# Performance work log

Measured on AMD Instinct MI355X. Metric: run time of the kernel, lower is better.

Reference implementation:

```python
import jax, jax.numpy as jnp
import numpy as np

B, S, D, H = 2, 2048, 2048, 16
HD = D // H  # head_dim = 128
ALIBI_BIAS_MAX = 8


def alibi_bias(n_heads, seq_len, alibi_bias_max=8, dtype=jnp.float32):
    # matches torch alibi_bias(full=False): shape [1, H, 1, S]
    dist = jnp.arange(1 - seq_len, 1, dtype=dtype).reshape(1, 1, 1, seq_len)
    m = jnp.arange(1, n_heads + 1, dtype=dtype) * (alibi_bias_max / n_heads)
    slopes = (1.0 / 2.0 ** m).reshape(1, n_heads, 1, 1)
    return dist * slopes


def setup_inputs() -> dict:
    key = jax.random.key(0)
    k1, k2, k3, k4, k5 = jax.random.split(key, 5)
    x = jax.random.normal(k1, (B, S, D), dtype=jnp.float32)
    # ALiBi additive bias, as produced by TritonFlashCausalAttention.attn_mask_
    attn_mask = alibi_bias(H, S, ALIBI_BIAS_MAX, jnp.float32)  # [1,H,1,S]
    scale = 1.0 / np.sqrt(D)
    Wqkv = jax.random.normal(k2, (D, 3 * D), dtype=jnp.float32) * scale
    bqkv = jnp.zeros((3 * D,), dtype=jnp.float32)
    Wout = jax.random.normal(k3, (D, D), dtype=jnp.float32) * scale
    bout = jnp.zeros((D,), dtype=jnp.float32)
    return {"x": x, "attn_mask": attn_mask, "Wqkv": Wqkv, "bqkv": bqkv,
            "Wout": Wout, "bout": bout}


def reference(x, attn_mask, Wqkv, bqkv, Wout, bout):
    b, s, d = x.shape
    # fused QKV projection
    qkv = x @ Wqkv + bqkv                       # [B,S,3D]
    qkv = qkv.reshape(b, s, 3, H, HD)
    q, k, v = qkv[:, :, 0], qkv[:, :, 1], qkv[:, :, 2]  # each [B,S,H,HD]
    softmax_scale = 1.0 / jnp.sqrt(jnp.asarray(HD, dtype=x.dtype))
    scores = jnp.einsum('bshd,bthd->bhst', q, k) * softmax_scale  # [B,H,S,S]
    scores = scores + attn_mask                  # ALiBi bias [1,H,1,S]
    causal = jnp.tril(jnp.ones((s, s), dtype=bool))
    scores = jnp.where(causal, scores, jnp.asarray(-jnp.inf, dtype=scores.dtype))
    attn = jax.nn.softmax(scores, axis=-1)
    out = jnp.einsum('bhst,bthd->bshd', attn, v).reshape(b, s, d)
    return out @ Wout + bout
```

## Files before the change

### kernel.cpp

```cpp
#include <hip/hip_runtime.h>
#include <hip/hip_bf16.h>

typedef __bf16 bf16x8 __attribute__((ext_vector_type(8)));
typedef float f32x4 __attribute__((ext_vector_type(4)));
typedef unsigned short u16;

constexpr int BATCH = 2, SEQ = 2048, DM = 2048, NH = 16, HD = 128;
constexpr int N3 = 3 * DM;
constexpr int MROWS = BATCH * SEQ;

__device__ __forceinline__ u16 f2bf(float f) {
  unsigned u = __builtin_bit_cast(unsigned, f);
  unsigned r = 0x7FFFu + ((u >> 16) & 1u);
  return (u16)((u + r) >> 16);
}

__device__ __forceinline__ void glds16(const u16* g, u16* l) {
  __builtin_amdgcn_global_load_lds(
      (const __attribute__((address_space(1))) unsigned*)(const void*)g,
      (__attribute__((address_space(3))) unsigned*)(void*)l, 16, 0, 0);
}

__global__ __launch_bounds__(256) void k_cvt(const float* __restrict__ in,
                                             u16* __restrict__ out, int n4) {
  int i = blockIdx.x * blockDim.x + threadIdx.x;
  if (i >= n4) return;
  float4 v = reinterpret_cast<const float4*>(in)[i];
  ushort4 o;
  o.x = f2bf(v.x); o.y = f2bf(v.y); o.z = f2bf(v.z); o.w = f2bf(v.w);
  reinterpret_cast<ushort4*>(out)[i] = o;
}

__global__ __launch_bounds__(256) void k_transpose(const float* __restrict__ in,
                                                   u16* __restrict__ out, int K, int N) {
  __shared__ float tile[32][33];
  int n0 = blockIdx.x * 32, k0 = blockIdx.y * 32;
  int tx = threadIdx.x & 31, ty = threadIdx.x >> 5;
#pragma unroll
  for (int r = ty; r < 32; r += 8) tile[r][tx] = in[(long)(k0 + r) * N + n0 + tx];
  __syncthreads();
#pragma unroll
  for (int r = ty; r < 32; r += 8) out[(long)(n0 + r) * K + k0 + tx] = f2bf(tile[tx][r]);
}

__global__ __launch_bounds__(256, 2) void k_gemm_qkv(const u16* __restrict__ A,
                                                     const u16* __restrict__ Bt,
                                                     const float* __restrict__ bias,
                                                     u16* __restrict__ Qb, u16* __restrict__ Kb,
                                                     u16* __restrict__ Vt) {
  constexpr int K = DM;
  constexpr int NKT = K / 64;
  constexpr int NIT = NKT / 2;
  __shared__ u16 LA[2 * 128 * 64];
  __shared__ u16 LB[2 * 192 * 64];
  int m0 = blockIdx.y * 128, n0 = blockIdx.x * 192;
  int t = threadIdx.x, lane = t & 63, w = t >> 6;
  int l15 = lane & 15, lhi = lane >> 4;
  int wrow = w >> 1, wcol = w & 1;
  int srow = t >> 3;
  int scol = ((t & 7) ^ (srow & 7)) * 8;

#define STG_A(TILE, IDX) do {                                                      \
    int kb_ = ((TILE) < NKT ? (TILE) : NKT - 1) * 64;                              \
    glds16(A + (long)(m0 + (IDX) * 32 + srow) * K + kb_ + scol,                    \
           LA + ((TILE) & 1) * 8192 + (IDX) * 2048 + w * 512);                     \
  } while (0)
#define STG_B(TILE, IDX) do {                                                      \
    int kb_ = ((TILE) < NKT ? (TILE) : NKT - 1) * 64;                              \
    glds16(Bt + (long)(n0 + (IDX) * 32 + srow) * K + kb_ + scol,                   \
           LB + ((TILE) & 1) * 12288 + (IDX) * 2048 + w * 512);                    \
  } while (0)

  bf16x8 af[2][2], bfr0[3][2], bfr1[3][2];
  f32x4 acc[4][6] = {};

#define LDA_FRAGS(BUF, QM) do {                                                    \
    _Pragma("unroll") for (int mi = 0; mi < 2; mi++) {                             \
      int rA = wrow * 64 + ((QM) * 2 + mi) * 16 + l15;                             \
      _Pragma("unroll") for (int kk = 0; kk < 2; kk++)                             \
        af[mi][kk] = *(const bf16x8*)(LA + (BUF) * 8192 + rA * 64 +                \
                                      (((kk * 4 + lhi) ^ (rA & 7)) * 8));          \
    } } while (0)
#define LDB_FRAGS(BUF, QN, DST) do {                                               \
    _Pragma("unroll") for (int ni = 0; ni < 3; ni++) {                             \
      int rB = wcol * 96 + ((QN) * 3 + ni) * 16 + l15;                             \
      _Pragma("unroll") for (int kk = 0; kk < 2; kk++)                             \
        DST[ni][kk] = *(const bf16x8*)(LB + (BUF) * 12288 + rB * 64 +              \
                                       (((kk * 4 + lhi) ^ (rB & 7)) * 8));         \
    } } while (0)
#define MM(QM, QN, BF) do {                                                        \
    __builtin_amdgcn_s_setprio(1);                                                 \
    _Pragma("unroll") for (int mi = 0; mi < 2; mi++)                               \
    _Pragma("unroll") for (int ni = 0; ni < 3; ni++)                               \
    _Pragma("unroll") for (int kk = 0; kk < 2; kk++)                               \
      acc[(QM) * 2 + mi][(QN) * 3 + ni] = __builtin_amdgcn_mfma_f32_16x16x32_bf16( \
          af[mi][kk], BF[ni][kk], acc[(QM) * 2 + mi][(QN) * 3 + ni], 0, 0, 0);     \
    __builtin_amdgcn_s_setprio(0);                                                 \
  } while (0)
#define BAR __builtin_amdgcn_s_barrier()
#define LG0 do { asm volatile("s_waitcnt lgkmcnt(0)" ::: "memory");                \
                 __builtin_amdgcn_sched_barrier(0); } while (0)
#define VMW6 do { asm volatile("s_waitcnt vmcnt(6)" ::: "memory");                 \
                  __builtin_amdgcn_sched_barrier(0); } while (0)

  STG_A(0, 0); STG_A(0, 1); STG_A(0, 2); STG_A(0, 3);
  STG_B(0, 0); STG_B(0, 1); STG_B(0, 2); STG_B(0, 3); STG_B(0, 4); STG_B(0, 5);
  STG_B(1, 0); STG_B(1, 1); STG_B(1, 2); STG_B(1, 3); STG_B(1, 4); STG_B(1, 5);
  VMW6; BAR;

  for (int it = 0; it < NIT; it++) {
    int k1 = 2 * it + 1, k2 = 2 * it + 2, k3 = 2 * it + 3;
    LDA_FRAGS(0, 0); LDB_FRAGS(0, 0, bfr0);
    STG_A(k1, 0); STG_A(k1, 1); STG_A(k1, 2);      BAR; LG0; MM(0, 0, bfr0); BAR;
    LDB_FRAGS(0, 1, bfr1);
    STG_A(k1, 3);                                  BAR; LG0; MM(0, 1, bfr1); BAR;
    LDA_FRAGS(0, 1);
    STG_B(k2, 0); STG_B(k2, 1); STG_B(k2, 2);      BAR; LG0; MM(1, 0, bfr0); BAR;
    STG_B(k2, 3); STG_B(k2, 4); STG_B(k2, 5);
    VMW6;                                          BAR;      MM(1, 1, bfr1); BAR;
    LDA_FRAGS(1, 0); LDB_FRAGS(1, 0, bfr0);
    STG_A(k2, 0); STG_A(k2, 1); STG_A(k2, 2);      BAR; LG0; MM(0, 0, bfr0); BAR;
    LDB_FRAGS(1, 1, bfr1);
    STG_A(k2, 3);                                  BAR; LG0; MM(0, 1, bfr1); BAR;
    LDA_FRAGS(1, 1);
    STG_B(k3, 0); STG_B(k3, 1); STG_B(k3, 2);      BAR; LG0; MM(1, 0, bfr0); BAR;
    STG_B(k3, 3); STG_B(k3, 4); STG_B(k3, 5);
    VMW6;                                          BAR;      MM(1, 1, bfr1); BAR;
  }
#undef STG_A
#undef STG_B
#undef LDA_FRAGS
#undef LDB_FRAGS
#undef MM
#undef BAR
#undef LG0
#undef VMW6

#pragma unroll
  for (int mi = 0; mi < 4; mi++)
#pragma unroll
    for (int ni = 0; ni < 6; ni++) {
      int col = n0 + wcol * 96 + ni * 16 + l15;
      float bv = bias[col];
      int sec = col >> 11, dn = col & 2047, h = dn >> 7, hd = dn & 127;
#pragma unroll
      for (int r = 0; r < 4; r++) {
        int row = m0 + wrow * 64 + mi * 16 + lhi * 4 + r;
        int bb = row >> 11, ss = row & 2047;
        u16 val = f2bf(acc[mi][ni][r] + bv);
        if (sec == 0)
          Qb[(((long)(bb * NH + h)) * SEQ + ss) * HD + hd] = val;
        else if (sec == 1)
          Kb[(((long)(bb * NH + h)) * SEQ + ss) * HD + hd] = val;
        else
          Vt[(((long)(bb * NH + h)) * HD + hd) * SEQ + ss] = val;
      }
    }
}

__global__ __launch_bounds__(256) void k_gemm_out(const u16* __restrict__ A,
                                                  const u16* __restrict__ Bt,
                                                  const float* __restrict__ bias,
                                                  float* __restrict__ Out) {
  constexpr int K = DM, N = DM;
  __shared__ u16 As[128 * 32], Bs[128 * 32];
  int m0 = blockIdx.y * 128, n0 = blockIdx.x * 128;
  int t = threadIdx.x, lane = t & 63, w = t >> 6;
  int l15 = lane & 15, lhi = lane >> 4;
  int wr = (w >> 1) * 64, wc = (w & 1) * 64;
  int srow = t >> 2, sk = (t & 3) * 8;
  const u16* Ap0 = A + (long)(m0 + srow) * K + sk;
  const u16* Ap1 = A + (long)(m0 + 64 + srow) * K + sk;
  const u16* Bp0 = Bt + (long)(n0 + srow) * K + sk;
  const u16* Bp1 = Bt + (long)(n0 + 64 + srow) * K + sk;
  u16* AsW0 = As + w * 512; u16* AsW1 = As + 2048 + w * 512;
  u16* BsW0 = Bs + w * 512; u16* BsW1 = Bs + 2048 + w * 512;

  f32x4 acc[4][4] = {};
  for (int k0 = 0; k0 < K; k0 += 32) {
    glds16(Ap0 + k0, AsW0);
    glds16(Ap1 + k0, AsW1);
    glds16(Bp0 + k0, BsW0);
    glds16(Bp1 + k0, BsW1);
    __syncthreads();
    bf16x8 af[4], bg[4];
#pragma unroll
    for (int i = 0; i < 4; i++) af[i] = *(const bf16x8*)(As + (wr + i * 16 + l15) * 32 + lhi * 8);
#pragma unroll
    for (int j = 0; j < 4; j++) bg[j] = *(const bf16x8*)(Bs + (wc + j * 16 + l15) * 32 + lhi * 8);
#pragma unroll
    for (int i = 0; i < 4; i++)
#pragma unroll
      for (int j = 0; j < 4; j++)
        acc[i][j] = __builtin_amdgcn_mfma_f32_16x16x32_bf16(af[i], bg[j], acc[i][j], 0, 0, 0);
    __syncthreads();
  }
#pragma unroll
  for (int i = 0; i < 4; i++)
#pragma unroll
    for (int j = 0; j < 4; j++) {
      int col = n0 + wc + j * 16 + l15;
      float bv = bias[col];
#pragma unroll
      for (int r = 0; r < 4; r++) {
        int row = m0 + wr + i * 16 + lhi * 4 + r;
        Out[(long)row * N + col] = acc[i][j][r] + bv;
      }
    }
}

__global__ __launch_bounds__(256) void k_attn(const u16* __restrict__ Qb,
                                              const u16* __restrict__ Kb,
                                              const u16* __restrict__ Vt,
                                              const float* __restrict__ mask,
                                              u16* __restrict__ Ao) {
  constexpr int NT = SEQ / 64;
  int bh = blockIdx.y;
  int qp = blockIdx.x;
  int t = threadIdx.x, w = t >> 6, lane = t & 63;
  int l15 = lane & 15, lhi = lane >> 4;
  int b = bh >> 4, h = bh & 15;
  const u16* Qh = Qb + (long)bh * SEQ * HD;
  const u16* Kh = Kb + (long)bh * SEQ * HD;
  const u16* Vh = Vt + (long)bh * HD * SEQ;
  const float* mh = mask + h * SEQ;

  __shared__ u16 Ks[64 * 128];
  __shared__ u16 Vs[128 * 64];
  __shared__ u16 p_lds[4 * 16 * 64];
  u16* pw = p_lds + w * (16 * 64);

  int krow[4], kcol[4], vrow[4], vcol[4];
#pragma unroll
  for (int i = 0; i < 4; i++) {
    int c = i * 256 + t;
    krow[i] = c >> 4; kcol[i] = (c & 15) * 8;
    vrow[i] = c >> 3; vcol[i] = (c & 7) * 8;
  }

  const float sm_scale = 0.08838834764831845f;

  for (int half = 0; half < 2; half++) {
    int qt = half ? qp : (NT - 1 - qp);
    int q0 = qt * 64 + w * 16;
    int nt = qt + 1;

    bf16x8 qf[4];
#pragma unroll
    for (int kc = 0; kc < 4; kc++)
      qf[kc] = *(const bf16x8*)(Qh + (long)(q0 + l15) * HD + kc * 32 + lhi * 8);

    int rowr[4];
#pragma unroll
    for (int r = 0; r < 4; r++) rowr[r] = q0 + lhi * 4 + r;

    float mrun[4], lrun[4];
    f32x4 oacc[8] = {};
#pragma unroll
    for (int r = 0; r < 4; r++) { mrun[r] = -1e30f; lrun[r] = 0.f; }

    bf16x8 kst[4], vst[4];
#pragma unroll
    for (int i = 0; i < 4; i++) kst[i] = *(const bf16x8*)(Kh + (long)krow[i] * HD + kcol[i]);
#pragma unroll
    for (int i = 0; i < 4; i++) vst[i] = *(const bf16x8*)(Vh + (long)vrow[i] * SEQ + vcol[i]);
    __syncthreads();
#pragma unroll
    for (int i = 0; i < 4; i++)
      *(bf16x8*)(Ks + krow[i] * 128 + (kcol[i] ^ ((krow[i] & 7) << 3))) = kst[i];
#pragma unroll
    for (int i = 0; i < 4; i++)
      *(bf16x8*)(Vs + vrow[i] * 64 + (vcol[i] ^ ((vrow[i] & 7) << 3))) = vst[i];
    __syncthreads();

    for (int kt = 0; kt < nt; kt++) {
      int kb = kt * 64;
      bool have_next = (kt + 1 < nt);
      bool diag = (kt == nt - 1);
      if (have_next) {
        int kb2 = kb + 64;
#pragma unroll
        for (int i = 0; i < 4; i++)
          kst[i] = *(const bf16x8*)(Kh + (long)(kb2 + krow[i]) * HD + kcol[i]);
#pragma unroll
        for (int i = 0; i < 4; i++)
          vst[i] = *(const bf16x8*)(Vh + (long)vrow[i] * SEQ + kb2 + vcol[i]);
      }
      float bvv[4];
#pragma unroll
      for (int cb = 0; cb < 4; cb++) bvv[cb] = mh[kb + cb * 16 + l15];
      f32x4 sc[4] = {};
      __builtin_amdgcn_s_setprio(1);
#pragma unroll
      for (int kc = 0; kc < 4; kc++)
#pragma unroll
        for (int cb = 0; cb < 4; cb++) {
          int rr = cb * 16 + l15;
          bf16x8 kf = *(const bf16x8*)(Ks + rr * 128 + ((kc * 32 + lhi * 8) ^ ((rr & 7) << 3)));
          sc[cb] = __builtin_amdgcn_mfma_f32_16x16x32_bf16(qf[kc], kf, sc[cb], 0, 0, 0);
        }
      __builtin_amdgcn_s_setprio(0);
      float p[4][4], tmax[4];
#pragma unroll
      for (int cb = 0; cb < 4; cb++) {
        int col = kb + cb * 16 + l15;
#pragma unroll
        for (int r = 0; r < 4; r++) {
          float v = sc[cb][r] * sm_scale + bvv[cb];
          if (diag) v = (col <= rowr[r]) ? v : -1e30f;
          p[cb][r] = v;
        }
      }
#pragma unroll
      for (int r = 0; r < 4; r++)
        tmax[r] = fmaxf(fmaxf(p[0][r], p[1][r]), fmaxf(p[2][r], p[3][r]));
      float alpha[4];
#pragma unroll
      for (int r = 0; r < 4; r++) {
        float v = tmax[r];
        v = fmaxf(v, __shfl_xor(v, 1));
        v = fmaxf(v, __shfl_xor(v, 2));
        v = fmaxf(v, __shfl_xor(v, 4));
        v = fmaxf(v, __shfl_xor(v, 8));
        float mnew = fmaxf(mrun[r], v);
        alpha[r] = __expf(mrun[r] - mnew);
        mrun[r] = mnew;
        float s = 0.f;
#pragma unroll
        for (int cb = 0; cb < 4; cb++) {
          float e = __expf(p[cb][r] - mnew);
          p[cb][r] = e;
          s += e;
        }
        s += __shfl_xor(s, 1); s += __shfl_xor(s, 2);
        s += __shfl_xor(s, 4); s += __shfl_xor(s, 8);
        lrun[r] = lrun[r] * alpha[r] + s;
      }
#pragma unroll
      for (int nb = 0; nb < 8; nb++)
#pragma unroll
        for (int r = 0; r < 4; r++) oacc[nb][r] *= alpha[r];
#pragma unroll
      for (int cb = 0; cb < 4; cb++)
#pragma unroll
        for (int r = 0; r < 4; r++) {
          int rr = lhi * 4 + r;
          pw[(rr * 64 + cb * 16 + l15) ^ ((rr & 7) << 3)] = f2bf(p[cb][r]);
        }
      asm volatile("s_waitcnt lgkmcnt(0)" ::: "memory");
      bf16x8 pa0 = *(const bf16x8*)(pw + ((l15 * 64 + lhi * 8) ^ ((l15 & 7) << 3)));
      bf16x8 pa1 = *(const bf16x8*)(pw + ((l15 * 64 + 32 + lhi * 8) ^ ((l15 & 7) << 3)));
      __builtin_amdgcn_s_setprio(1);
#pragma unroll
      for (int nb = 0; nb < 8; nb++) {
        int rr = nb * 16 + l15;
        bf16x8 vf0 = *(const bf16x8*)(Vs + rr * 64 + ((lhi * 8) ^ ((rr & 7) << 3)));
        bf16x8 vf1 = *(const bf16x8*)(Vs + rr * 64 + ((32 + lhi * 8) ^ ((rr & 7) << 3)));
        oacc[nb] = __builtin_amdgcn_mfma_f32_16x16x32_bf16(pa0, vf0, oacc[nb], 0, 0, 0);
        oacc[nb] = __builtin_amdgcn_mfma_f32_16x16x32_bf16(pa1, vf1, oacc[nb], 0, 0, 0);
      }
      __builtin_amdgcn_s_setprio(0);
      if (have_next) {
        __syncthreads();
#pragma unroll
        for (int i = 0; i < 4; i++)
          *(bf16x8*)(Ks + krow[i] * 128 + (kcol[i] ^ ((krow[i] & 7) << 3))) = kst[i];
#pragma unroll
        for (int i = 0; i < 4; i++)
          *(bf16x8*)(Vs + vrow[i] * 64 + (vcol[i] ^ ((vrow[i] & 7) << 3))) = vst[i];
        __syncthreads();
      }
    }
#pragma unroll
    for (int nb = 0; nb < 8; nb++)
#pragma unroll
      for (int r = 0; r < 4; r++) {
        int row = q0 + lhi * 4 + r;
        float v = oacc[nb][r] / lrun[r];
        Ao[((long)(b * SEQ + row)) * DM + h * HD + nb * 16 + l15] = f2bf(v);
      }
  }
}

extern "C" void kernel_launch(void* const* d_in, const int* in_sizes, int n_in,
                              void* d_out, int out_size, void* d_ws, size_t ws_size,
                              hipStream_t stream) {
  const float* x    = (const float*)d_in[0];
  const float* amsk = (const float*)d_in[1];
  const float* Wqkv = (const float*)d_in[2];
  const float* bqkv = (const float*)d_in[3];
  const float* Wout = (const float*)d_in[4];
  const float* bout = (const float*)d_in[5];
  float* out = (float*)d_out;

  char* ws = (char*)d_ws;
  u16* xb  = (u16*)(ws + 0);
  u16* WqT = (u16*)(ws + 16777216UL);
  u16* WoT = (u16*)(ws + 41943040UL);
  u16* Qb  = (u16*)(ws + 50331648UL);
  u16* Kb  = (u16*)(ws + 67108864UL);
  u16* Vt  = (u16*)(ws + 83886080UL);
  u16* Ao  = (u16*)(ws + 100663296UL);

  k_cvt<<<8192, 256, 0, stream>>>(x, xb, (MROWS * DM) / 4);
  k_transpose<<<dim3(N3 / 32, DM / 32), 256, 0, stream>>>(Wqkv, WqT, DM, N3);
  k_transpose<<<dim3(DM / 32, DM / 32), 256, 0, stream>>>(Wout, WoT, DM, DM);
  k_gemm_qkv<<<dim3(N3 / 192, MROWS / 128), 256, 0, stream>>>(xb, WqT, bqkv, Qb, Kb, Vt);
  k_attn<<<dim3(SEQ / 128, BATCH * NH), 256, 0, stream>>>(Qb, Kb, Vt, amsk, Ao);
  k_gemm_out<<<dim3(DM / 128, MROWS / 128), 256, 0, stream>>>(Ao, WoT, bout, out);
}
```

Baseline: 296.3 us.

## Split attention KV loop across two wave groups with final softmax merge

The attention kernel now launches 512 threads per block, organised as two groups of four waves. Each group processes alternate 64-key tiles into its own K/V shared buffers, which splits the sequential KV loop for each query tile in half. At the end, group 1 writes its partial output, max and sum to shared memory, and group 0 merges the two online-softmax states before writing. The goal is more parallelism per block, since the grid has only 512 blocks. The cost is double the shared memory, extra barriers, and merge overhead. Occupancy may also be limited by launch_bounds(512,4) register pressure.

```diff
diff --git a/kernel.cpp b/kernel.cpp
--- a/kernel.cpp
+++ b/kernel.cpp
@@ -209,31 +209,35 @@
     }
 }
 
-__global__ __launch_bounds__(256) void k_attn(const u16* __restrict__ Qb,
-                                              const u16* __restrict__ Kb,
-                                              const u16* __restrict__ Vt,
-                                              const float* __restrict__ mask,
-                                              u16* __restrict__ Ao) {
+__global__ __launch_bounds__(512, 4) void k_attn(const u16* __restrict__ Qb,
+                                                 const u16* __restrict__ Kb,
+                                                 const u16* __restrict__ Vt,
+                                                 const float* __restrict__ mask,
+                                                 u16* __restrict__ Ao) {
   constexpr int NT = SEQ / 64;
   int bh = blockIdx.y;
   int qp = blockIdx.x;
   int t = threadIdx.x, w = t >> 6, lane = t & 63;
+  int g = w >> 2, wi = w & 3;
   int l15 = lane & 15, lhi = lane >> 4;
+  int tg = t & 255;
   int b = bh >> 4, h = bh & 15;
   const u16* Qh = Qb + (long)bh * SEQ * HD;
   const u16* Kh = Kb + (long)bh * SEQ * HD;
   const u16* Vh = Vt + (long)bh * HD * SEQ;
   const float* mh = mask + h * SEQ;
 
-  __shared__ u16 Ks[64 * 128];
-  __shared__ u16 Vs[128 * 64];
-  __shared__ u16 p_lds[4 * 16 * 64];
+  __shared__ u16 Ks[2][64 * 128];
+  __shared__ u16 Vs[2][128 * 64];
+  __shared__ u16 p_lds[8 * 16 * 64];
   u16* pw = p_lds + w * (16 * 64);
+  u16* Ksg = Ks[g];
+  u16* Vsg = Vs[g];
 
   int krow[4], kcol[4], vrow[4], vcol[4];
 #pragma unroll
   for (int i = 0; i < 4; i++) {
-    int c = i * 256 + t;
+    int c = i * 256 + tg;
     krow[i] = c >> 4; kcol[i] = (c & 15) * 8;
     vrow[i] = c >> 3; vcol[i] = (c & 7) * 8;
   }
@@ -242,43 +246,46 @@
 
   for (int half = 0; half < 2; half++) {
     int qt = half ? qp : (NT - 1 - qp);
-    int q0 = qt * 64 + w * 16;
+    int q0 = qt * 64 + wi * 16;
     int nt = qt + 1;
+    int nIt = (nt + 1) >> 1;
 
     bf16x8 qf[4];
 #pragma unroll
     for (int kc = 0; kc < 4; kc++)
       qf[kc] = *(const bf16x8*)(Qh + (long)(q0 + l15) * HD + kc * 32 + lhi * 8);
 
-    int rowr[4];
-#pragma unroll
-    for (int r = 0; r < 4; r++) rowr[r] = q0 + lhi * 4 + r;
-
     float mrun[4], lrun[4];
     f32x4 oacc[8] = {};
 #pragma unroll
     for (int r = 0; r < 4; r++) { mrun[r] = -1e30f; lrun[r] = 0.f; }
 
     bf16x8 kst[4], vst[4];
-#pragma unroll
-    for (int i = 0; i < 4; i++) kst[i] = *(const bf16x8*)(Kh + (long)krow[i] * HD + kcol[i]);
-#pragma unroll
-    for (int i = 0; i < 4; i++) vst[i] = *(const bf16x8*)(Vh + (long)vrow[i] * SEQ + vcol[i]);
-    __syncthreads();
-#pragma unroll
-    for (int i = 0; i < 4; i++)
-      *(bf16x8*)(Ks + krow[i] * 128 + (kcol[i] ^ ((krow[i] & 7) << 3))) = kst[i];
-#pragma unroll
-    for (int i = 0; i < 4; i++)
-      *(bf16x8*)(Vs + vrow[i] * 64 + (vcol[i] ^ ((vrow[i] & 7) << 3))) = vst[i];
-    __syncthreads();
-
-    for (int kt = 0; kt < nt; kt++) {
+    if (g < nt) {
+      int kb0 = g * 64;
+#pragma unroll
+      for (int i = 0; i < 4; i++) kst[i] = *(const bf16x8*)(Kh + (long)(kb0 + krow[i]) * HD + kcol[i]);
+#pragma unroll
+      for (int i = 0; i < 4; i++) vst[i] = *(const bf16x8*)(Vh + (long)vrow[i] * SEQ + kb0 + vcol[i]);
+    }
+    __syncthreads();
+    if (g < nt) {
+#pragma unroll
+      for (int i = 0; i < 4; i++)
+        *(bf16x8*)(Ksg + krow[i] * 128 + (kcol[i] ^ ((krow[i] & 7) << 3))) = kst[i];
+#pragma unroll
+      for (int i = 0; i < 4; i++)
+        *(bf16x8*)(Vsg + vrow[i] * 64 + (vcol[i] ^ ((vrow[i] & 7) << 3))) = vst[i];
+    }
+    __syncthreads();
+
+    for (int it = 0; it < nIt; it++) {
+      int kt = 2 * it + g;
+      bool active = kt < nt;
       int kb = kt * 64;
-      bool have_next = (kt + 1 < nt);
-      bool diag = (kt == nt - 1);
-      if (have_next) {
-        int kb2 = kb + 64;
+      bool havenext = (kt + 2) < nt;
+      if (havenext) {
+        int kb2 = kb + 128;
 #pragma unroll
         for (int i = 0; i < 4; i++)
           kst[i] = *(const bf16x8*)(Kh + (long)(kb2 + krow[i]) * HD + kcol[i]);
@@ -286,99 +293,134 @@
         for (int i = 0; i < 4; i++)
           vst[i] = *(const bf16x8*)(Vh + (long)vrow[i] * SEQ + kb2 + vcol[i]);
       }
-      float bvv[4];
-#pragma unroll
-      for (int cb = 0; cb < 4; cb++) bvv[cb] = mh[kb + cb * 16 + l15];
-      f32x4 sc[4] = {};
-      __builtin_amdgcn_s_setprio(1);
-#pragma unroll
-      for (int kc = 0; kc < 4; kc++)
+      if (active) {
+        bool diag = (kt == nt - 1);
+        float bvv[4];
+#pragma unroll
+        for (int cb = 0; cb < 4; cb++) bvv[cb] = mh[kb + cb * 16 + l15];
+        f32x4 sc[4] = {};
+        __builtin_amdgcn_s_setprio(1);
+#pragma unroll
+        for (int kc = 0; kc < 4; kc++)
+#pragma unroll
+          for (int cb = 0; cb < 4; cb++) {
+            int rr = cb * 16 + l15;
+            bf16x8 kf = *(const bf16x8*)(Ksg + rr * 128 + ((kc * 32 + lhi * 8) ^ ((rr & 7) << 3)));
+            sc[cb] = __builtin_amdgcn_mfma_f32_16x16x32_bf16(qf[kc], kf, sc[cb], 0, 0, 0);
+          }
+        __builtin_amdgcn_s_setprio(0);
+        float p[4][4], tmax[4];
 #pragma unroll
         for (int cb = 0; cb < 4; cb++) {
-          int rr = cb * 16 + l15;
-          bf16x8 kf = *(const bf16x8*)(Ks + rr * 128 + ((kc * 32 + lhi * 8) ^ ((rr & 7) << 3)));
-          sc[cb] = __builtin_amdgcn_mfma_f32_16x16x32_bf16(qf[kc], kf, sc[cb], 0, 0, 0);
-        }
-      __builtin_amdgcn_s_setprio(0);
-      float p[4][4], tmax[4];
-#pragma unroll
-      for (int cb = 0; cb < 4; cb++) {
-        int col = kb + cb * 16 + l15;
+          int col = kb + cb * 16 + l15;
+#pragma unroll
+          for (int r = 0; r < 4; r++) {
+            float v = sc[cb][r] * sm_scale + bvv[cb];
+            if (diag) v = (col <= q0 + lhi * 4 + r) ? v : -1e30f;
+            p[cb][r] = v;
+          }
+        }
+#pragma unroll
+        for (int r = 0; r < 4; r++)
+          tmax[r] = fmaxf(fmaxf(p[0][r], p[1][r]), fmaxf(p[2][r], p[3][r]));
+        float alpha[4];
 #pragma unroll
         for (int r = 0; r < 4; r++) {
-          float v = sc[cb][r] * sm_scale + bvv[cb];
-          if (diag) v = (col <= rowr[r]) ? v : -1e30f;
-          p[cb][r] = v;
-        }
-      }
-#pragma unroll
-      for (int r = 0; r < 4; r++)
-        tmax[r] = fmaxf(fmaxf(p[0][r], p[1][r]), fmaxf(p[2][r], p[3][r]));
-      float alpha[4];
+          float v = tmax[r];
+          v = fmaxf(v, __shfl_xor(v, 1));
+          v = fmaxf(v, __shfl_xor(v, 2));
+          v = fmaxf(v, __shfl_xor(v, 4));
+          v = fmaxf(v, __shfl_xor(v, 8));
+          float mnew = fmaxf(mrun[r], v);
+          alpha[r] = __expf(mrun[r] - mnew);
+          mrun[r] = mnew;
+          float s = 0.f;
+#pragma unroll
+          for (int cb = 0; cb < 4; cb++) {
+            float e = __expf(p[cb][r] - mnew);
+            p[cb][r] = e;
+            s += e;
+          }
+          s += __shfl_xor(s, 1); s += __shfl_xor(s, 2);
+          s += __shfl_xor(s, 4); s += __shfl_xor(s, 8);
+          lrun[r] = lrun[r] * alpha[r] + s;
+        }
+#pragma unroll
+        for (int nb = 0; nb < 8; nb++)
+#pragma unroll
+          for (int r = 0; r < 4; r++) oacc[nb][r] *= alpha[r];
+#pragma unroll
+        for (int cb = 0; cb < 4; cb++)
+#pragma unroll
+          for (int r = 0; r < 4; r++) {
+            int rr = lhi * 4 + r;
+            pw[(rr * 64 + cb * 16 + l15) ^ ((rr & 7) << 3)] = f2bf(p[cb][r]);
+          }
+        asm volatile("s_waitcnt lgkmcnt(0)" ::: "memory");
+        bf16x8 pa0 = *(const bf16x8*)(pw + ((l15 * 64 + lhi * 8) ^ ((l15 & 7) << 3)));
+        bf16x8 pa1 = *(const bf16x8*)(pw + ((l15 * 64 + 32 + lhi * 8) ^ ((l15 & 7) << 3)));
+        __builtin_amdgcn_s_setprio(1);
+#pragma unroll
+        for (int nb = 0; nb < 8; nb++) {
+          int rr = nb * 16 + l15;
+          bf16x8 vf0 = *(const bf16x8*)(Vsg + rr * 64 + ((lhi * 8) ^ ((rr & 7) << 3)));
+          bf16x8 vf1 = *(const bf16x8*)(Vsg + rr * 64 + ((32 + lhi * 8) ^ ((rr & 7) << 3)));
+          oacc[nb] = __builtin_amdgcn_mfma_f32_16x16x32_bf16(pa0, vf0, oacc[nb], 0, 0, 0);
+          oacc[nb] = __builtin_amdgcn_mfma_f32_16x16x32_bf16(pa1, vf1, oacc[nb], 0, 0, 0);
+        }
+        __builtin_amdgcn_s_setprio(0);
+      }
+      if (it + 1 < nIt) {
+        __syncthreads();
+        if (havenext) {
+#pragma unroll
+          for (int i = 0; i < 4; i++)
+            *(bf16x8*)(Ksg + krow[i] * 128 + (kcol[i] ^ ((krow[i] & 7) << 3))) = kst[i];
+#pragma unroll
+          for (int i = 0; i < 4; i++)
+            *(bf16x8*)(Vsg + vrow[i] * 64 + (vcol[i] ^ ((vrow[i] & 7) << 3))) = vst[i];
+        }
+        __syncthreads();
+      }
+    }
+
+    __syncthreads();
+    float* KsF = (float*)&Ks[0][0];
+    float* plF = (float*)p_lds;
+    if (g == 1) {
+#pragma unroll
+      for (int nb = 0; nb < 8; nb++)
+#pragma unroll
+        for (int r = 0; r < 4; r++)
+          KsF[wi * 2048 + (lhi * 4 + r) * 128 + nb * 16 + l15] = oacc[nb][r];
+      if (l15 == 0) {
+#pragma unroll
+        for (int r = 0; r < 4; r++) {
+          plF[wi * 32 + (lhi * 4 + r) * 2 + 0] = mrun[r];
+          plF[wi * 32 + (lhi * 4 + r) * 2 + 1] = lrun[r];
+        }
+      }
+    }
+    __syncthreads();
+    if (g == 0) {
 #pragma unroll
       for (int r = 0; r < 4; r++) {
-        float v = tmax[r];
-        v = fmaxf(v, __shfl_xor(v, 1));
-        v = fmaxf(v, __shfl_xor(v, 2));
-        v = fmaxf(v, __shfl_xor(v, 4));
-        v = fmaxf(v, __shfl_xor(v, 8));
-        float mnew = fmaxf(mrun[r], v);
-        alpha[r] = __expf(mrun[r] - mnew);
-        mrun[r] = mnew;
-        float s = 0.f;
-#pragma unroll
-        for (int cb = 0; cb < 4; cb++) {
-          float e = __expf(p[cb][r] - mnew);
-          p[cb][r] = e;
-          s += e;
-        }
-        s += __shfl_xor(s, 1); s += __shfl_xor(s, 2);
-        s += __shfl_xor(s, 4); s += __shfl_xor(s, 8);
-        lrun[r] = lrun[r] * alpha[r] + s;
-      }
-#pragma unroll
-      for (int nb = 0; nb < 8; nb++)
-#pragma unroll
-        for (int r = 0; r < 4; r++) oacc[nb][r] *= alpha[r];
-#pragma unroll
-      for (int cb = 0; cb < 4; cb++)
-#pragma unroll
-        for (int r = 0; r < 4; r++) {
-          int rr = lhi * 4 + r;
-          pw[(rr * 64 + cb * 16 + l15) ^ ((rr & 7) << 3)] = f2bf(p[cb][r]);
-        }
-      asm volatile("s_waitcnt lgkmcnt(0)" ::: "memory");
-      bf16x8 pa0 = *(const bf16x8*)(pw + ((l15 * 64 + lhi * 8) ^ ((l15 & 7) << 3)));
-      bf16x8 pa1 = *(const bf16x8*)(pw + ((l15 * 64 + 32 + lhi * 8) ^ ((l15 & 7) << 3)));
-      __builtin_amdgcn_s_setprio(1);
-#pragma unroll
-      for (int nb = 0; nb < 8; nb++) {
-        int rr = nb * 16 + l15;
-        bf16x8 vf0 = *(const bf16x8*)(Vs + rr * 64 + ((lhi * 8) ^ ((rr & 7) << 3)));
-        bf16x8 vf1 = *(const bf16x8*)(Vs + rr * 64 + ((32 + lhi * 8) ^ ((rr & 7) << 3)));
-        oacc[nb] = __builtin_amdgcn_mfma_f32_16x16x32_bf16(pa0, vf0, oacc[nb], 0, 0, 0);
-        oacc[nb] = __builtin_amdgcn_mfma_f32_16x16x32_bf16(pa1, vf1, oacc[nb], 0, 0, 0);
-      }
-      __builtin_amdgcn_s_setprio(0);
-      if (have_next) {
-        __syncthreads();
-#pragma unroll
-        for (int i = 0; i < 4; i++)
-          *(bf16x8*)(Ks + krow[i] * 128 + (kcol[i] ^ ((krow[i] & 7) << 3))) = kst[i];
-#pragma unroll
-        for (int i = 0; i < 4; i++)
-          *(bf16x8*)(Vs + vrow[i] * 64 + (vcol[i] ^ ((vrow[i] & 7) << 3))) = vst[i];
-        __syncthreads();
-      }
-    }
-#pragma unroll
-    for (int nb = 0; nb < 8; nb++)
-#pragma unroll
-      for (int r = 0; r < 4; r++) {
-        int row = q0 + lhi * 4 + r;
-        float v = oacc[nb][r] / lrun[r];
-        Ao[((long)(b * SEQ + row)) * DM + h * HD + nb * 16 + l15] = f2bf(v);
-      }
+        int rr = lhi * 4 + r;
+        float m1 = plF[wi * 32 + rr * 2 + 0];
+        float l1 = plF[wi * 32 + rr * 2 + 1];
+        float mm = fmaxf(mrun[r], m1);
+        float a0 = __expf(mrun[r] - mm);
+        float a1 = __expf(m1 - mm);
+        float linv = 1.f / (lrun[r] * a0 + l1 * a1);
+        int row = q0 + rr;
+#pragma unroll
+        for (int nb = 0; nb < 8; nb++) {
+          float o1 = KsF[wi * 2048 + rr * 128 + nb * 16 + l15];
+          float v = (oacc[nb][r] * a0 + o1 * a1) * linv;
+          Ao[((long)(b * SEQ + row)) * DM + h * HD + nb * 16 + l15] = f2bf(v);
+        }
+      }
+    }
   }
 }
 
@@ -406,6 +448,6 @@
   k_transpose<<<dim3(N3 / 32, DM / 32), 256, 0, stream>>>(Wqkv, WqT, DM, N3);
   k_transpose<<<dim3(DM / 32, DM / 32), 256, 0, stream>>>(Wout, WoT, DM, DM);
   k_gemm_qkv<<<dim3(N3 / 192, MROWS / 128), 256, 0, stream>>>(xb, WqT, bqkv, Qb, Kb, Vt);
-  k_attn<<<dim3(SEQ / 128, BATCH * NH), 256, 0, stream>>>(Qb, Kb, Vt, amsk, Ao);
+  k_attn<<<dim3(SEQ / 128, BATCH * NH), 512, 0, stream>>>(Qb, Kb, Vt, amsk, Ao);
   k_gemm_out<<<dim3(DM / 128, MROWS / 128), 256, 0, stream>>>(Ao, WoT, bout, out);
 }
```

Measured after the change: 509.8 us. 72.1% more time.

## Pipeline output GEMM with double-buffered swizzled LDS and interleaved MFMA phases

Applied to the files above, without the earlier changes.

Rewrites the output projection GEMM to use 64-wide K tiles in double-buffered LDS, with XOR-swizzled layout to avoid bank conflicts. Global-to-LDS loads for the next tiles are issued in between quadrant MFMA phases, using explicit vmcnt/lgkmcnt waits, barriers and setprio, so memory traffic overlaps compute. It also sets launch bounds to two blocks per CU. The cost is more LDS per block, tight manual scheduling, and more barriers per iteration.

```diff
diff --git a/kernel.cpp b/kernel.cpp
--- a/kernel.cpp
+++ b/kernel.cpp
@@ -158,53 +158,108 @@
     }
 }
 
-__global__ __launch_bounds__(256) void k_gemm_out(const u16* __restrict__ A,
-                                                  const u16* __restrict__ Bt,
-                                                  const float* __restrict__ bias,
-                                                  float* __restrict__ Out) {
+__global__ __launch_bounds__(256, 2) void k_gemm_out(const u16* __restrict__ A,
+                                                     const u16* __restrict__ Bt,
+                                                     const float* __restrict__ bias,
+                                                     float* __restrict__ Out) {
   constexpr int K = DM, N = DM;
-  __shared__ u16 As[128 * 32], Bs[128 * 32];
+  constexpr int NKT = K / 64;
+  constexpr int NIT = NKT / 2;
+  __shared__ u16 LA[2 * 128 * 64];
+  __shared__ u16 LB[2 * 128 * 64];
   int m0 = blockIdx.y * 128, n0 = blockIdx.x * 128;
   int t = threadIdx.x, lane = t & 63, w = t >> 6;
   int l15 = lane & 15, lhi = lane >> 4;
-  int wr = (w >> 1) * 64, wc = (w & 1) * 64;
-  int srow = t >> 2, sk = (t & 3) * 8;
-  const u16* Ap0 = A + (long)(m0 + srow) * K + sk;
-  const u16* Ap1 = A + (long)(m0 + 64 + srow) * K + sk;
-  const u16* Bp0 = Bt + (long)(n0 + srow) * K + sk;
-  const u16* Bp1 = Bt + (long)(n0 + 64 + srow) * K + sk;
-  u16* AsW0 = As + w * 512; u16* AsW1 = As + 2048 + w * 512;
-  u16* BsW0 = Bs + w * 512; u16* BsW1 = Bs + 2048 + w * 512;
-
+  int wrow = w >> 1, wcol = w & 1;
+  int srow = t >> 3;
+  int scol = ((t & 7) ^ (srow & 7)) * 8;
+
+#define STG_A(TILE, IDX) do {                                                      \
+    int kb_ = ((TILE) < NKT ? (TILE) : NKT - 1) * 64;                              \
+    glds16(A + (long)(m0 + (IDX) * 32 + srow) * K + kb_ + scol,                    \
+           LA + ((TILE) & 1) * 8192 + (IDX) * 2048 + w * 512);                     \
+  } while (0)
+#define STG_B(TILE, IDX) do {                                                      \
+    int kb_ = ((TILE) < NKT ? (TILE) : NKT - 1) * 64;                              \
+    glds16(Bt + (long)(n0 + (IDX) * 32 + srow) * K + kb_ + scol,                   \
+           LB + ((TILE) & 1) * 8192 + (IDX) * 2048 + w * 512);                     \
+  } while (0)
+
+  bf16x8 af[2][2], bfr0[2][2], bfr1[2][2];
   f32x4 acc[4][4] = {};
-  for (int k0 = 0; k0 < K; k0 += 32) {
-    glds16(Ap0 + k0, AsW0);
-    glds16(Ap1 + k0, AsW1);
-    glds16(Bp0 + k0, BsW0);
-    glds16(Bp1 + k0, BsW1);
-    __syncthreads();
-    bf16x8 af[4], bg[4];
-#pragma unroll
-    for (int i = 0; i < 4; i++) af[i] = *(const bf16x8*)(As + (wr + i * 16 + l15) * 32 + lhi * 8);
-#pragma unroll
-    for (int j = 0; j < 4; j++) bg[j] = *(const bf16x8*)(Bs + (wc + j * 16 + l15) * 32 + lhi * 8);
-#pragma unroll
-    for (int i = 0; i < 4; i++)
-#pragma unroll
-      for (int j = 0; j < 4; j++)
-        acc[i][j] = __builtin_amdgcn_mfma_f32_16x16x32_bf16(af[i], bg[j], acc[i][j], 0, 0, 0);
-    __syncthreads();
+
+#define LDA_FRAGS(BUF, QM) do {                                                    \
+    _Pragma("unroll") for (int mi = 0; mi < 2; mi++) {                             \
+      int rA = wrow * 64 + ((QM) * 2 + mi) * 16 + l15;                             \
+      _Pragma("unroll") for (int kk = 0; kk < 2; kk++)                             \
+        af[mi][kk] = *(const bf16x8*)(LA + (BUF) * 8192 + rA * 64 +                \
+                                      (((kk * 4 + lhi) ^ (rA & 7)) * 8));          \
+    } } while (0)
+#define LDB_FRAGS(BUF, QN, DST) do {                                               \
+    _Pragma("unroll") for (int ni = 0; ni < 2; ni++) {                             \
+      int rB = wcol * 64 + ((QN) * 2 + ni) * 16 + l15;                             \
+      _Pragma("unroll") for (int kk = 0; kk < 2; kk++)                             \
+        DST[ni][kk] = *(const bf16x8*)(LB + (BUF) * 8192 + rB * 64 +               \
+                                       (((kk * 4 + lhi) ^ (rB & 7)) * 8));         \
+    } } while (0)
+#define MM(QM, QN, BF) do {                                                        \
+    __builtin_amdgcn_s_setprio(1);                                                 \
+    _Pragma("unroll") for (int mi = 0; mi < 2; mi++)                               \
+    _Pragma("unroll") for (int ni = 0; ni < 2; ni++)                               \
+    _Pragma("unroll") for (int kk = 0; kk < 2; kk++)                               \
+      acc[(QM) * 2 + mi][(QN) * 2 + ni] = __builtin_amdgcn_mfma_f32_16x16x32_bf16( \
+          af[mi][kk], BF[ni][kk], acc[(QM) * 2 + mi][(QN) * 2 + ni], 0, 0, 0);     \
+    __builtin_amdgcn_s_setprio(0);                                                 \
+  } while (0)
+#define BAR __builtin_amdgcn_s_barrier()
+#define LG0 do { asm volatile("s_waitcnt lgkmcnt(0)" ::: "memory");                \
+                 __builtin_amdgcn_sched_barrier(0); } while (0)
+#define VMW4 do { asm volatile("s_waitcnt vmcnt(4)" ::: "memory");                 \
+                  __builtin_amdgcn_sched_barrier(0); } while (0)
+
+  STG_A(0, 0); STG_A(0, 1); STG_A(0, 2); STG_A(0, 3);
+  STG_B(0, 0); STG_B(0, 1); STG_B(0, 2); STG_B(0, 3);
+  STG_B(1, 0); STG_B(1, 1); STG_B(1, 2); STG_B(1, 3);
+  VMW4; BAR;
+
+  for (int it = 0; it < NIT; it++) {
+    int k1 = 2 * it + 1, k2 = 2 * it + 2, k3 = 2 * it + 3;
+    LDA_FRAGS(0, 0); LDB_FRAGS(0, 0, bfr0);
+    STG_A(k1, 0); STG_A(k1, 1); STG_A(k1, 2);      BAR; LG0; MM(0, 0, bfr0); BAR;
+    LDB_FRAGS(0, 1, bfr1);
+    STG_A(k1, 3);                                  BAR; LG0; MM(0, 1, bfr1); BAR;
+    LDA_FRAGS(0, 1);
+    STG_B(k2, 0); STG_B(k2, 1); STG_B(k2, 2);      BAR; LG0; MM(1, 0, bfr0); BAR;
+    STG_B(k2, 3);
+    VMW4;                                          BAR;      MM(1, 1, bfr1); BAR;
+    LDA_FRAGS(1, 0); LDB_FRAGS(1, 0, bfr0);
+    STG_A(k2, 0); STG_A(k2, 1); STG_A(k2, 2);      BAR; LG0; MM(0, 0, bfr0); BAR;
+    LDB_FRAGS(1, 1, bfr1);
+    STG_A(k2, 3);                                  BAR; LG0; MM(0, 1, bfr1); BAR;
+    LDA_FRAGS(1, 1);
+    STG_B(k3, 0); STG_B(k3, 1); STG_B(k3, 2);      BAR; LG0; MM(1, 0, bfr0); BAR;
+    STG_B(k3, 3);
+    VMW4;                                          BAR;      MM(1, 1, bfr1); BAR;
   }
-#pragma unroll
-  for (int i = 0; i < 4; i++)
-#pragma unroll
-    for (int j = 0; j < 4; j++) {
-      int col = n0 + wc + j * 16 + l15;
+#undef STG_A
+#undef STG_B
+#undef LDA_FRAGS
+#undef LDB_FRAGS
+#undef MM
+#undef BAR
+#undef LG0
+#undef VMW4
+
+#pragma unroll
+  for (int mi = 0; mi < 4; mi++)
+#pragma unroll
+    for (int ni = 0; ni < 4; ni++) {
+      int col = n0 + wcol * 64 + ni * 16 + l15;
       float bv = bias[col];
 #pragma unroll
       for (int r = 0; r < 4; r++) {
-        int row = m0 + wr + i * 16 + lhi * 4 + r;
-        Out[(long)row * N + col] = acc[i][j][r] + bv;
+        int row = m0 + wrow * 64 + mi * 16 + lhi * 4 + r;
+        Out[(long)row * N + col] = acc[mi][ni][r] + bv;
       }
     }
 }
```

Result: faster. 287.0 us (-3.1%).
